# Optimization experiments

Measured on AMD Instinct MI355X. Metric: run time of the kernel, lower is better.

Reference implementation:

```python
import jax, jax.numpy as jnp
import numpy as np

N, E, D, L = 50000, 800000, 128, 2
EPS = 1e-7

def _logmap0(y):
    # Poincare ball (c=1) logmap at origin: artanh(||y||) * y / ||y||
    n = jnp.linalg.norm(y, axis=-1, keepdims=True)
    nc = jnp.clip(n, EPS, 1.0 - 1e-5)
    return jnp.arctanh(nc) * y / jnp.maximum(n, EPS)

def _expmap0(u):
    # Poincare ball (c=1) expmap at origin: tanh(||u||) * u / ||u||
    n = jnp.linalg.norm(u, axis=-1, keepdims=True)
    return jnp.tanh(n) * u / jnp.maximum(n, EPS)

def _l2norm(x):
    # F.normalize(p=2, dim=1)
    return x / jnp.maximum(jnp.linalg.norm(x, axis=1, keepdims=True), 1e-12)

def setup_inputs() -> dict:
    key = jax.random.key(0)
    ks = jax.random.split(key, 12)
    src = jax.random.randint(ks[0], (E,), 0, N)
    dst = jax.random.randint(ks[1], (E,), 0, N)
    e_emb = jax.random.normal(ks[2], (N, D), jnp.float32)
    b_emb = jax.random.normal(ks[3], (N, D), jnp.float32) * 0.1  # inside Poincare ball
    s_emb = jax.random.normal(ks[4], (N, D), jnp.float32)
    sc = 0.05
    eW = jax.random.normal(ks[5], (L, D, D), jnp.float32) * sc
    eB = jax.random.normal(ks[6], (L, D), jnp.float32) * sc
    bW = jax.random.normal(ks[7], (L, D, D), jnp.float32) * sc
    bB = jax.random.normal(ks[8], (L, D), jnp.float32) * sc
    sW = jax.random.normal(ks[9], (L, D, D), jnp.float32) * sc
    sB = jax.random.normal(ks[10], (L, D), jnp.float32) * sc
    return dict(e_emb=e_emb, b_emb=b_emb, s_emb=s_emb, eW=eW, eB=eB,
                bW=bW, bB=bB, sW=sW, sB=sB, src=src, dst=dst)

def reference(e_emb, b_emb, s_emb, eW, eB, bW, bB, sW, sB, src, dst):
    n_nodes = e_emb.shape[0]
    ones_e = jnp.ones(src.shape[0], jnp.float32)
    in_deg = jax.ops.segment_sum(ones_e, dst, num_segments=n_nodes)
    out_deg = jax.ops.segment_sum(ones_e, src, num_segments=n_nodes)
    # DGL GraphConv norm='both': D_out^{-1/2} (sum over in-neighbors) D_in^{-1/2}
    norm_out = jnp.where(out_deg > 0, out_deg ** -0.5, 0.0)[:, None]
    norm_in = jnp.where(in_deg > 0, in_deg ** -0.5, 0.0)[:, None]
    inv_in = jnp.where(in_deg > 0, 1.0 / in_deg, 0.0)[:, None]  # mean reduce

    def agg_sum(h):
        return jax.ops.segment_sum(h[src], dst, num_segments=n_nodes)

    for l in range(L):
        # Euclidean branch: GraphConv(norm='both') then LeakyReLU(0.2)
        h = agg_sum(e_emb * norm_out) * norm_in
        e_emb = jax.nn.leaky_relu(h @ eW[l].T + eB[l], negative_slope=0.2)
        # Hyperbolic branch: logmap0 -> Linear -> neighbor mean -> expmap0
        tan_b = _logmap0(b_emb) @ bW[l].T + bB[l]
        b_emb = _expmap0(agg_sum(tan_b) * inv_in)
        # Spherical branch: normalize -> Linear -> neighbor mean -> normalize
        tan_s = _l2norm(s_emb) @ sW[l].T + sB[l]
        s_emb = _l2norm(agg_sum(tan_s) * inv_in)
    return (e_emb, b_emb, s_emb)
```

## Files before the change

### kernel.cpp

```cpp
#include <hip/hip_runtime.h>
#include <math.h>

#define DD 128
#define PSTRIDE 384

typedef _Float16 half8 __attribute__((ext_vector_type(8)));
typedef _Float16 half2v __attribute__((ext_vector_type(2)));
typedef float floatx4 __attribute__((ext_vector_type(4)));

__device__ __forceinline__ float wave_sum_f(float x) {
#pragma unroll
  for (int m = 32; m >= 1; m >>= 1) x += __shfl_xor(x, m, 64);
  return x;
}
__device__ __forceinline__ float g16_sum(float x) {
#pragma unroll
  for (int m = 8; m >= 1; m >>= 1) x += __shfl_xor(x, m, 64);
  return x;
}
__device__ __forceinline__ int wave_sum_i(int x) {
#pragma unroll
  for (int m = 32; m >= 1; m >>= 1) x += __shfl_xor(x, m, 64);
  return x;
}

__global__ void setup_fused_kernel(const int* __restrict__ src, const int* __restrict__ dst,
                                   int* __restrict__ out_deg, int* __restrict__ in_deg, int E,
                                   const float* __restrict__ e0, const float* __restrict__ b0,
                                   const float* __restrict__ s0, _Float16* __restrict__ P, int N,
                                   const float* __restrict__ eW, const float* __restrict__ bW,
                                   const float* __restrict__ sW, _Float16* __restrict__ Wh, int nW,
                                   int DB, int AB) {
  int bx = blockIdx.x;
  if (bx < DB) {
    int e = bx * 256 + threadIdx.x;
    if (e < E) {
      atomicAdd(&out_deg[src[e]], 1);
      atomicAdd(&in_deg[dst[e]], 1);
    }
  } else if (bx < DB + AB) {
    int lane = threadIdx.x & 63;
    int v = (bx - DB) * 4 + (threadIdx.x >> 6);
    if (v >= N) return;
    size_t ri = (size_t)v * 64 + lane;
    float2 e2 = ((const float2*)e0)[ri];
    float2 b2 = ((const float2*)b0)[ri];
    float2 s2 = ((const float2*)s0)[ri];
    float nb = sqrtf(wave_sum_f(b2.x * b2.x + b2.y * b2.y));
    float ns = sqrtf(wave_sum_f(s2.x * s2.x + s2.y * s2.y));
    float ncb = fminf(fmaxf(nb, 1e-7f), 1.0f - 1e-5f);
    float fb = atanhf(ncb) / fmaxf(nb, 1e-7f);
    float fs = 1.0f / fmaxf(ns, 1e-12f);
    _Float16* Pr = P + (size_t)v * PSTRIDE + lane * 2;
    half2v he; he.x = (_Float16)e2.x;        he.y = (_Float16)e2.y;
    half2v hb; hb.x = (_Float16)(b2.x * fb); hb.y = (_Float16)(b2.y * fb);
    half2v hs; hs.x = (_Float16)(s2.x * fs); hs.y = (_Float16)(s2.y * fs);
    *(half2v*)&Pr[0]   = he;
    *(half2v*)&Pr[128] = hb;
    *(half2v*)&Pr[256] = hs;
  } else {
    int i = (bx - DB - AB) * 256 + threadIdx.x;
    if (i < nW) {
      Wh[i]          = (_Float16)eW[i];
      Wh[i + nW]     = (_Float16)bW[i];
      Wh[i + 2 * nW] = (_Float16)sW[i];
    }
  }
}

__global__ void norms_psum_kernel(const int* __restrict__ in_deg, const int* __restrict__ out_deg,
                                  float* __restrict__ norm_in, float* __restrict__ norm_out,
                                  float* __restrict__ inv_in, int* __restrict__ part, int N) {
  __shared__ int wsum[4];
  int t = threadIdx.x, lane = t & 63, w = t >> 6;
  int i = blockIdx.x * 256 + t;
  int di = 0;
  if (i < N) {
    di = in_deg[i];
    int dq = out_deg[i];
    norm_in[i]  = di > 0 ? 1.0f / sqrtf((float)di) : 0.0f;
    norm_out[i] = dq > 0 ? 1.0f / sqrtf((float)dq) : 0.0f;
    inv_in[i]   = di > 0 ? 1.0f / (float)di : 0.0f;
  }
  int s = wave_sum_i(di);
  if (lane == 0) wsum[w] = s;
  __syncthreads();
  if (t == 0) part[blockIdx.x] = wsum[0] + wsum[1] + wsum[2] + wsum[3];
}

__global__ void part_scan_kernel(int* __restrict__ part, int nb) {
  __shared__ int wsum[4];
  int t = threadIdx.x, lane = t & 63, w = t >> 6;
  int x = (t < nb) ? part[t] : 0;
  int v = x;
#pragma unroll
  for (int off = 1; off < 64; off <<= 1) {
    int y = __shfl_up(v, off, 64);
    if (lane >= off) v += y;
  }
  if (lane == 63) wsum[w] = v;
  __syncthreads();
  int base = 0;
  for (int j = 0; j < w; ++j) base += wsum[j];
  if (t < nb) part[t] = base + v - x;
}

__global__ void local_scan_kernel(const int* __restrict__ deg, const int* __restrict__ part,
                                  int* __restrict__ row_off, int N, int E) {
  __shared__ int wsum[4];
  int t = threadIdx.x, lane = t & 63, w = t >> 6;
  int i = blockIdx.x * 256 + t;
  int x = (i < N) ? deg[i] : 0;
  int v = x;
#pragma unroll
  for (int off = 1; off < 64; off <<= 1) {
    int y = __shfl_up(v, off, 64);
    if (lane >= off) v += y;
  }
  if (lane == 63) wsum[w] = v;
  __syncthreads();
  int base = 0;
  for (int j = 0; j < w; ++j) base += wsum[j];
  if (i < N) row_off[i] = part[blockIdx.x] + base + v - x;
  if (blockIdx.x == 0 && t == 0) row_off[N] = E;
}

__device__ __forceinline__ void gemm_tile(int part, int rb, const _Float16* __restrict__ P,
                                          const _Float16* __restrict__ Wh,
                                          const float* __restrict__ Bb,
                                          _Float16* __restrict__ Q, int N) {
  int t = threadIdx.x, lane = t & 63, w = t >> 6;
  int m = lane & 15, quad = lane >> 4, c0 = w * 32;
  int rbase = rb * 64;
  const _Float16* Ain = P + part * DD;
  _Float16* Qo = Q + part * DD;
  half8 bf[2][4];
#pragma unroll
  for (int tj = 0; tj < 2; ++tj)
#pragma unroll
    for (int kk = 0; kk < 4; ++kk)
      bf[tj][kk] = *(const half8*)&Wh[(c0 + tj * 16 + m) * DD + kk * 32 + quad * 8];
  float bias0 = 0.f, bias1 = 0.f;
  if (Bb) { bias0 = Bb[c0 + m]; bias1 = Bb[c0 + 16 + m]; }
#pragma unroll
  for (int r = 0; r < 4; ++r) {
    int row0 = r * 16;
    int arow = rbase + row0 + m; if (arow >= N) arow = N - 1;
    const _Float16* Ap = Ain + (size_t)arow * PSTRIDE;
    floatx4 acc0 = {0.f, 0.f, 0.f, 0.f}, acc1 = {0.f, 0.f, 0.f, 0.f};
#pragma unroll
    for (int kk = 0; kk < 4; ++kk) {
      half8 af = *(const half8*)&Ap[kk * 32 + quad * 8];
      acc0 = __builtin_amdgcn_mfma_f32_16x16x32_f16(af, bf[0][kk], acc0, 0, 0, 0);
      acc1 = __builtin_amdgcn_mfma_f32_16x16x32_f16(af, bf[1][kk], acc1, 0, 0, 0);
    }
    int vrow = rbase + row0 + quad * 4;
#pragma unroll
    for (int reg = 0; reg < 4; ++reg) {
      int v = vrow + reg;
      if (v < N) {
        Qo[(size_t)v * PSTRIDE + c0 + m]      = (_Float16)(acc0[reg] + bias0);
        Qo[(size_t)v * PSTRIDE + c0 + 16 + m] = (_Float16)(acc1[reg] + bias1);
      }
    }
  }
}

__global__ __launch_bounds__(256) void fill_gemm_kernel(
    const int* __restrict__ src, const int* __restrict__ dst,
    const float* __restrict__ norm_out, const int* __restrict__ row_off,
    int* __restrict__ cursor, int2* __restrict__ csr_sw, int E,
    const _Float16* __restrict__ P, const _Float16* __restrict__ WhE,
    const _Float16* __restrict__ WhB, const _Float16* __restrict__ WhS,
    const float* __restrict__ bBl, const float* __restrict__ sBl,
    _Float16* __restrict__ Q, int N, int FB, int GB) {
  int bx = blockIdx.x;
  if (bx < FB) {
    int e = bx * 256 + threadIdx.x;
    if (e < E) {
      int d = dst[e], s = src[e];
      int pos = row_off[d] + atomicAdd(&cursor[d], 1);
      csr_sw[pos] = make_int2(s, __float_as_int(norm_out[s]));
    }
  } else {
    int gb = bx - FB;
    int part = gb / GB, rb = gb % GB;
    const _Float16* Wh = (part == 0) ? WhE : (part == 1 ? WhB : WhS);
    const float* Bb = (part == 0) ? nullptr : (part == 1 ? bBl : sBl);
    gemm_tile(part, rb, P, Wh, Bb, Q, N);
  }
}

__global__ __launch_bounds__(256) void gemm3_kernel(const _Float16* __restrict__ P,
                                                    const _Float16* __restrict__ WhE,
                                                    const _Float16* __restrict__ WhB,
                                                    const _Float16* __restrict__ WhS,
                                                    const float* __restrict__ bBl,
                                                    const float* __restrict__ sBl,
                                                    _Float16* __restrict__ Q, int N) {
  int part = blockIdx.y;
  const _Float16* Wh = (part == 0) ? WhE : (part == 1 ? WhB : WhS);
  const float* Bb = (part == 0) ? nullptr : (part == 1 ? bBl : sBl);
  gemm_tile(part, blockIdx.x, P, Wh, Bb, Q, N);
}

__global__ __launch_bounds__(256) void agg_fused_kernel(
    const _Float16* __restrict__ Q, const int* __restrict__ row_off,
    const int2* __restrict__ csr_sw, const float* __restrict__ norm_in,
    const float* __restrict__ inv_in, const float* __restrict__ eBias,
    float* __restrict__ oe, float* __restrict__ ob, float* __restrict__ os,
    _Float16* __restrict__ Pnext, int N, int write_pack, int write_out) {
  int lane = threadIdx.x & 63;
  int v = blockIdx.x * 4 + (threadIdx.x >> 6);
  if (v >= N) return;
  int g = lane >> 4, q = lane & 15;
  int beg = row_off[v], end = row_off[v + 1];
  float eacc[8], bacc[8], sacc[8];
#pragma unroll
  for (int j = 0; j < 8; ++j) { eacc[j] = 0.f; bacc[j] = 0.f; sacc[j] = 0.f; }
  int i = beg;
  for (; i + 8 <= end; i += 8) {
    int2 swa = csr_sw[i + g];
    int2 swb = csr_sw[i + 4 + g];
    float wa = __int_as_float(swa.y), wb = __int_as_float(swb.y);
    const _Float16* ra = Q + (size_t)swa.x * PSTRIDE + q * 8;
    const _Float16* rb = Q + (size_t)swb.x * PSTRIDE + q * 8;
    half8 ea = *(const half8*)ra;
    half8 e2 = *(const half8*)rb;
    half8 ba = *(const half8*)(ra + 128);
    half8 b2 = *(const half8*)(rb + 128);
    half8 sa = *(const half8*)(ra + 256);
    half8 s2 = *(const half8*)(rb + 256);
#pragma unroll
    for (int j = 0; j < 8; ++j) {
      eacc[j] += wa * (float)ea[j];
      eacc[j] += wb * (float)e2[j];
      bacc[j] += (float)ba[j];
      bacc[j] += (float)b2[j];
      sacc[j] += (float)sa[j];
      sacc[j] += (float)s2[j];
    }
  }
  if (i + 4 <= end) {
    int2 sw = csr_sw[i + g];
    float wgt = __int_as_float(sw.y);
    const _Float16* rp = Q + (size_t)sw.x * PSTRIDE + q * 8;
    half8 ev = *(const half8*)rp;
    half8 bv = *(const half8*)(rp + 128);
    half8 sv = *(const half8*)(rp + 256);
#pragma unroll
    for (int j = 0; j < 8; ++j) {
      eacc[j] += wgt * (float)ev[j];
      bacc[j] += (float)bv[j];
      sacc[j] += (float)sv[j];
    }
    i += 4;
  }
  if (i + g < end) {
    int2 sw = csr_sw[i + g];
    float wgt = __int_as_float(sw.y);
    const _Float16* rp = Q + (size_t)sw.x * PSTRIDE + q * 8;
    half8 ev = *(const half8*)rp;
    half8 bv = *(const half8*)(rp + 128);
    half8 sv = *(const half8*)(rp + 256);
#pragma unroll
    for (int j = 0; j < 8; ++j) {
      eacc[j] += wgt * (float)ev[j];
      bacc[j] += (float)bv[j];
      sacc[j] += (float)sv[j];
    }
  }
#pragma unroll
  for (int j = 0; j < 8; ++j) {
    eacc[j] += __shfl_xor(eacc[j], 16, 64);
    eacc[j] += __shfl_xor(eacc[j], 32, 64);
    bacc[j] += __shfl_xor(bacc[j], 16, 64);
    bacc[j] += __shfl_xor(bacc[j], 32, 64);
    sacc[j] += __shfl_xor(sacc[j], 16, 64);
    sacc[j] += __shfl_xor(sacc[j], 32, 64);
  }
  float ni = norm_in[v], iv = inv_in[v];
  const float4* ebp = (const float4*)eBias;
  float4 eb0 = ebp[q * 2], eb1 = ebp[q * 2 + 1];
  float bias[8] = {eb0.x, eb0.y, eb0.z, eb0.w, eb1.x, eb1.y, eb1.z, eb1.w};
  float h[8], ub[8], us[8];
  float ss2 = 0.f;
#pragma unroll
  for (int j = 0; j < 8; ++j) {
    float t = eacc[j] * ni + bias[j];
    h[j] = t > 0.f ? t : 0.2f * t;
    ub[j] = bacc[j] * iv;
    us[j] = sacc[j] * iv; ss2 += us[j] * us[j];
  }
  float ns = sqrtf(g16_sum(ss2));
  float fs = 1.0f / fmaxf(ns, 1e-12f);
  if (write_out) {
    float bs2 = 0.f;
#pragma unroll
    for (int j = 0; j < 8; ++j) bs2 += ub[j] * ub[j];
    float nb = sqrtf(g16_sum(bs2));
    float fb = tanhf(nb) / fmaxf(nb, 1e-7f);
    if (g == 0) {
      float4* p = (float4*)(oe + (size_t)v * DD);
      p[q * 2]     = make_float4(h[0], h[1], h[2], h[3]);
      p[q * 2 + 1] = make_float4(h[4], h[5], h[6], h[7]);
    } else if (g == 1) {
      float4* p = (float4*)(ob + (size_t)v * DD);
      p[q * 2]     = make_float4(ub[0] * fb, ub[1] * fb, ub[2] * fb, ub[3] * fb);
      p[q * 2 + 1] = make_float4(ub[4] * fb, ub[5] * fb, ub[6] * fb, ub[7] * fb);
    } else if (g == 2) {
      float4* p = (float4*)(os + (size_t)v * DD);
      p[q * 2]     = make_float4(us[0] * fs, us[1] * fs, us[2] * fs, us[3] * fs);
      p[q * 2 + 1] = make_float4(us[4] * fs, us[5] * fs, us[6] * fs, us[7] * fs);
    }
  }
  if (write_pack) {
    if (g == 3) {
      half8 he, hb, hs;
#pragma unroll
      for (int j = 0; j < 8; ++j) {
        he[j] = (_Float16)h[j];
        hb[j] = (_Float16)ub[j];
        hs[j] = (_Float16)(us[j] * fs);
      }
      _Float16* Pr = Pnext + (size_t)v * PSTRIDE + q * 8;
      *(half8*)&Pr[0]   = he;
      *(half8*)&Pr[128] = hb;
      *(half8*)&Pr[256] = hs;
    }
  }
}

extern "C" void kernel_launch(void* const* d_in, const int* in_sizes, int n_in,
                              void* d_out, int out_size, void* d_ws, size_t ws_size,
                              hipStream_t stream) {
  const float* e0 = (const float*)d_in[0];
  const float* b0 = (const float*)d_in[1];
  const float* s0 = (const float*)d_in[2];
  const float* eW = (const float*)d_in[3];
  const float* eB = (const float*)d_in[4];
  const float* bW = (const float*)d_in[5];
  const float* bB = (const float*)d_in[6];
  const float* sW = (const float*)d_in[7];
  const float* sB = (const float*)d_in[8];
  const int* src = (const int*)d_in[9];
  const int* dst = (const int*)d_in[10];
  int N = in_sizes[0] / DD;
  int E = in_sizes[9];
  int L = in_sizes[3] / (DD * DD);
  int LDD2 = L * DD * DD;

  char* w = (char*)d_ws;
  int* in_deg  = (int*)w; w += (size_t)N * 4;
  int* out_deg = (int*)w; w += (size_t)N * 4;
  int* cursor  = (int*)w; w += (size_t)N * 4;
  int* row_off = (int*)w; w += (size_t)(N + 4) * 4;
  int* pscan   = (int*)w; w += (size_t)1024 * 4;
  int2* csr_sw = (int2*)w; w += (size_t)E * 8;
  float* norm_in  = (float*)w; w += (size_t)N * 4;
  float* norm_out = (float*)w; w += (size_t)N * 4;
  float* inv_in   = (float*)w; w += (size_t)N * 4;
  w = (char*)(((size_t)w + 255) & ~(size_t)255);
  _Float16* P = (_Float16*)w; w += (size_t)N * PSTRIDE * 2;
  _Float16* Q = (_Float16*)w; w += (size_t)N * PSTRIDE * 2;
  _Float16* Wh = (_Float16*)w; w += (size_t)3 * LDD2 * 2;
  _Float16* whE = Wh;
  _Float16* whB = Wh + LDD2;
  _Float16* whS = Wh + 2 * LDD2;

  float* oe = (float*)d_out;
  float* ob = oe + (size_t)N * DD;
  float* os = ob + (size_t)N * DD;

  int DB = (E + 255) / 256;
  int AB = (N + 3) / 4;
  int GB = (N + 63) / 64;
  int WB = (LDD2 + 255) / 256;
  int PB = (N + 255) / 256;

  hipMemsetAsync(d_ws, 0, (size_t)3 * N * 4, stream);
  setup_fused_kernel<<<DB + AB + WB, 256, 0, stream>>>(src, dst, out_deg, in_deg, E,
                                                       e0, b0, s0, P, N,
                                                       eW, bW, sW, Wh, LDD2, DB, AB);
  norms_psum_kernel<<<PB, 256, 0, stream>>>(in_deg, out_deg, norm_in, norm_out, inv_in, pscan, N);
  part_scan_kernel<<<1, 256, 0, stream>>>(pscan, PB);
  local_scan_kernel<<<PB, 256, 0, stream>>>(in_deg, pscan, row_off, N, E);
  fill_gemm_kernel<<<DB + 3 * GB, 256, 0, stream>>>(src, dst, norm_out, row_off, cursor, csr_sw, E,
                                                    P, whE, whB, whS, bB, sB, Q, N, DB, GB);
  agg_fused_kernel<<<AB, 256, 0, stream>>>(Q, row_off, csr_sw, norm_in, inv_in, eB,
                                           oe, ob, os, P, N,
                                           (L > 1) ? 1 : 0, (L == 1) ? 1 : 0);
  for (int l = 1; l < L; ++l) {
    size_t lo = (size_t)l * DD * DD;
    gemm3_kernel<<<dim3(GB, 3), 256, 0, stream>>>(P, whE + lo, whB + lo, whS + lo,
                                                  bB + (size_t)l * DD, sB + (size_t)l * DD, Q, N);
    agg_fused_kernel<<<AB, 256, 0, stream>>>(Q, row_off, csr_sw, norm_in, inv_in,
                                             eB + (size_t)l * DD, oe, ob, os, P, N,
                                             (l < L - 1) ? 1 : 0, (l == L - 1) ? 1 : 0);
  }
}
```

Baseline: 496.2 us.

## Fuse layer-0 input prep into GEMM and spread degree atomics over 8 copies

The separate pass that converted the fp32 inputs to fp16 and applied logmap0 or l2 normalisation into P is removed. The first GEMM now reads fp32 rows directly, computes each row's norm inside the tile, and applies the per-row scale to the MFMA output before the bias. Degree counting now spreads atomics across 8 histogram copies chosen by wave index, and the norms kernel sums those copies. This cuts a full-size read and write pass and atomic contention, at the cost of a larger memset and more fp32 loads in the GEMM.

```diff
diff --git a/kernel.cpp b/kernel.cpp
--- a/kernel.cpp
+++ b/kernel.cpp
@@ -5,61 +5,35 @@
 #define PSTRIDE 384
 
 typedef _Float16 half8 __attribute__((ext_vector_type(8)));
-typedef _Float16 half2v __attribute__((ext_vector_type(2)));
 typedef float floatx4 __attribute__((ext_vector_type(4)));
 
-__device__ __forceinline__ float wave_sum_f(float x) {
+__device__ __forceinline__ float g16_sum(float x) {
+#pragma unroll
+  for (int m = 8; m >= 1; m >>= 1) x += __shfl_xor(x, m, 64);
+  return x;
+}
+__device__ __forceinline__ int wave_sum_i(int x) {
 #pragma unroll
   for (int m = 32; m >= 1; m >>= 1) x += __shfl_xor(x, m, 64);
   return x;
 }
-__device__ __forceinline__ float g16_sum(float x) {
-#pragma unroll
-  for (int m = 8; m >= 1; m >>= 1) x += __shfl_xor(x, m, 64);
-  return x;
-}
-__device__ __forceinline__ int wave_sum_i(int x) {
-#pragma unroll
-  for (int m = 32; m >= 1; m >>= 1) x += __shfl_xor(x, m, 64);
-  return x;
-}
-
-__global__ void setup_fused_kernel(const int* __restrict__ src, const int* __restrict__ dst,
-                                   int* __restrict__ out_deg, int* __restrict__ in_deg, int E,
-                                   const float* __restrict__ e0, const float* __restrict__ b0,
-                                   const float* __restrict__ s0, _Float16* __restrict__ P, int N,
-                                   const float* __restrict__ eW, const float* __restrict__ bW,
-                                   const float* __restrict__ sW, _Float16* __restrict__ Wh, int nW,
-                                   int DB, int AB) {
+
+__global__ void deg_wcvt_kernel(const int* __restrict__ src, const int* __restrict__ dst,
+                                int* __restrict__ out_deg8, int* __restrict__ in_deg8,
+                                int E, int N,
+                                const float* __restrict__ eW, const float* __restrict__ bW,
+                                const float* __restrict__ sW, _Float16* __restrict__ Wh, int nW,
+                                int DB) {
   int bx = blockIdx.x;
   if (bx < DB) {
     int e = bx * 256 + threadIdx.x;
     if (e < E) {
-      atomicAdd(&out_deg[src[e]], 1);
-      atomicAdd(&in_deg[dst[e]], 1);
-    }
-  } else if (bx < DB + AB) {
-    int lane = threadIdx.x & 63;
-    int v = (bx - DB) * 4 + (threadIdx.x >> 6);
-    if (v >= N) return;
-    size_t ri = (size_t)v * 64 + lane;
-    float2 e2 = ((const float2*)e0)[ri];
-    float2 b2 = ((const float2*)b0)[ri];
-    float2 s2 = ((const float2*)s0)[ri];
-    float nb = sqrtf(wave_sum_f(b2.x * b2.x + b2.y * b2.y));
-    float ns = sqrtf(wave_sum_f(s2.x * s2.x + s2.y * s2.y));
-    float ncb = fminf(fmaxf(nb, 1e-7f), 1.0f - 1e-5f);
-    float fb = atanhf(ncb) / fmaxf(nb, 1e-7f);
-    float fs = 1.0f / fmaxf(ns, 1e-12f);
-    _Float16* Pr = P + (size_t)v * PSTRIDE + lane * 2;
-    half2v he; he.x = (_Float16)e2.x;        he.y = (_Float16)e2.y;
-    half2v hb; hb.x = (_Float16)(b2.x * fb); hb.y = (_Float16)(b2.y * fb);
-    half2v hs; hs.x = (_Float16)(s2.x * fs); hs.y = (_Float16)(s2.y * fs);
-    *(half2v*)&Pr[0]   = he;
-    *(half2v*)&Pr[128] = hb;
-    *(half2v*)&Pr[256] = hs;
+      int h = ((bx << 2) + (threadIdx.x >> 6)) & 7;
+      atomicAdd(&out_deg8[h * N + src[e]], 1);
+      atomicAdd(&in_deg8[h * N + dst[e]], 1);
+    }
   } else {
-    int i = (bx - DB - AB) * 256 + threadIdx.x;
+    int i = (bx - DB) * 256 + threadIdx.x;
     if (i < nW) {
       Wh[i]          = (_Float16)eW[i];
       Wh[i + nW]     = (_Float16)bW[i];
@@ -68,16 +42,22 @@
   }
 }
 
-__global__ void norms_psum_kernel(const int* __restrict__ in_deg, const int* __restrict__ out_deg,
-                                  float* __restrict__ norm_in, float* __restrict__ norm_out,
-                                  float* __restrict__ inv_in, int* __restrict__ part, int N) {
+__global__ void norms_psum_kernel(const int* __restrict__ in_deg8, const int* __restrict__ out_deg8,
+                                  int* __restrict__ in_deg, float* __restrict__ norm_in,
+                                  float* __restrict__ norm_out, float* __restrict__ inv_in,
+                                  int* __restrict__ part, int N) {
   __shared__ int wsum[4];
   int t = threadIdx.x, lane = t & 63, w = t >> 6;
   int i = blockIdx.x * 256 + t;
   int di = 0;
   if (i < N) {
-    di = in_deg[i];
-    int dq = out_deg[i];
+    int dq = 0;
+#pragma unroll
+    for (int h = 0; h < 8; ++h) {
+      di += in_deg8[h * N + i];
+      dq += out_deg8[h * N + i];
+    }
+    in_deg[i] = di;
     norm_in[i]  = di > 0 ? 1.0f / sqrtf((float)di) : 0.0f;
     norm_out[i] = dq > 0 ? 1.0f / sqrtf((float)dq) : 0.0f;
     inv_in[i]   = di > 0 ? 1.0f / (float)di : 0.0f;
@@ -123,6 +103,72 @@
   for (int j = 0; j < w; ++j) base += wsum[j];
   if (i < N) row_off[i] = part[blockIdx.x] + base + v - x;
   if (blockIdx.x == 0 && t == 0) row_off[N] = E;
+}
+
+__device__ __forceinline__ void gemm0_tile(int part, int rb, const float* __restrict__ A,
+                                           const _Float16* __restrict__ Wh,
+                                           const float* __restrict__ Bb,
+                                           _Float16* __restrict__ Q, int N) {
+  int t = threadIdx.x, lane = t & 63, w = t >> 6;
+  int m = lane & 15, quad = lane >> 4, c0 = w * 32;
+  int rbase = rb * 64;
+  _Float16* Qo = Q + part * DD;
+  half8 bf[2][4];
+#pragma unroll
+  for (int tj = 0; tj < 2; ++tj)
+#pragma unroll
+    for (int kk = 0; kk < 4; ++kk)
+      bf[tj][kk] = *(const half8*)&Wh[(c0 + tj * 16 + m) * DD + kk * 32 + quad * 8];
+  float bias0 = 0.f, bias1 = 0.f;
+  if (part) { bias0 = Bb[c0 + m]; bias1 = Bb[c0 + 16 + m]; }
+#pragma unroll
+  for (int r = 0; r < 4; ++r) {
+    int row0 = r * 16;
+    int arow = rbase + row0 + m; if (arow >= N) arow = N - 1;
+    const float* Ap = A + (size_t)arow * DD;
+    half8 af[4];
+    float nsq = 0.f;
+#pragma unroll
+    for (int kk = 0; kk < 4; ++kk) {
+      float4 x0 = *(const float4*)&Ap[kk * 32 + quad * 8];
+      float4 x1 = *(const float4*)&Ap[kk * 32 + quad * 8 + 4];
+      if (part)
+        nsq += x0.x * x0.x + x0.y * x0.y + x0.z * x0.z + x0.w * x0.w +
+               x1.x * x1.x + x1.y * x1.y + x1.z * x1.z + x1.w * x1.w;
+      half8 a;
+      a[0] = (_Float16)x0.x; a[1] = (_Float16)x0.y; a[2] = (_Float16)x0.z; a[3] = (_Float16)x0.w;
+      a[4] = (_Float16)x1.x; a[5] = (_Float16)x1.y; a[6] = (_Float16)x1.z; a[7] = (_Float16)x1.w;
+      af[kk] = a;
+    }
+    float fr = 1.f;
+    if (part) {
+      nsq += __shfl_xor(nsq, 16, 64);
+      nsq += __shfl_xor(nsq, 32, 64);
+      float n = sqrtf(nsq);
+      if (part == 1) {
+        float nc = fminf(fmaxf(n, 1e-7f), 1.0f - 1e-5f);
+        fr = atanhf(nc) / fmaxf(n, 1e-7f);
+      } else {
+        fr = 1.0f / fmaxf(n, 1e-12f);
+      }
+    }
+    floatx4 acc0 = {0.f, 0.f, 0.f, 0.f}, acc1 = {0.f, 0.f, 0.f, 0.f};
+#pragma unroll
+    for (int kk = 0; kk < 4; ++kk) {
+      acc0 = __builtin_amdgcn_mfma_f32_16x16x32_f16(af[kk], bf[0][kk], acc0, 0, 0, 0);
+      acc1 = __builtin_amdgcn_mfma_f32_16x16x32_f16(af[kk], bf[1][kk], acc1, 0, 0, 0);
+    }
+    int vrow = rbase + row0 + quad * 4;
+#pragma unroll
+    for (int reg = 0; reg < 4; ++reg) {
+      int v = vrow + reg;
+      float fs = part ? __shfl(fr, quad * 4 + reg, 64) : 1.f;
+      if (v < N) {
+        Qo[(size_t)v * PSTRIDE + c0 + m]      = (_Float16)(acc0[reg] * fs + bias0);
+        Qo[(size_t)v * PSTRIDE + c0 + 16 + m] = (_Float16)(acc1[reg] * fs + bias1);
+      }
+    }
+  }
 }
 
 __device__ __forceinline__ void gemm_tile(int part, int rb, const _Float16* __restrict__ P,
@@ -166,14 +212,14 @@
   }
 }
 
-__global__ __launch_bounds__(256) void fill_gemm_kernel(
+__global__ __launch_bounds__(256) void fill_gemm0_kernel(
     const int* __restrict__ src, const int* __restrict__ dst,
     const float* __restrict__ norm_out, const int* __restrict__ row_off,
     int* __restrict__ cursor, int2* __restrict__ csr_sw, int E,
-    const _Float16* __restrict__ P, const _Float16* __restrict__ WhE,
-    const _Float16* __restrict__ WhB, const _Float16* __restrict__ WhS,
-    const float* __restrict__ bBl, const float* __restrict__ sBl,
-    _Float16* __restrict__ Q, int N, int FB, int GB) {
+    const float* __restrict__ e0, const float* __restrict__ b0, const float* __restrict__ s0,
+    const _Float16* __restrict__ WhE, const _Float16* __restrict__ WhB,
+    const _Float16* __restrict__ WhS, const float* __restrict__ bBl,
+    const float* __restrict__ sBl, _Float16* __restrict__ Q, int N, int FB, int GB) {
   int bx = blockIdx.x;
   if (bx < FB) {
     int e = bx * 256 + threadIdx.x;
@@ -185,9 +231,10 @@
   } else {
     int gb = bx - FB;
     int part = gb / GB, rb = gb % GB;
+    const float* A = (part == 0) ? e0 : (part == 1 ? b0 : s0);
     const _Float16* Wh = (part == 0) ? WhE : (part == 1 ? WhB : WhS);
     const float* Bb = (part == 0) ? nullptr : (part == 1 ? bBl : sBl);
-    gemm_tile(part, rb, P, Wh, Bb, Q, N);
+    gemm0_tile(part, rb, A, Wh, Bb, Q, N);
   }
 }
 
@@ -351,12 +398,13 @@
   int LDD2 = L * DD * DD;
 
   char* w = (char*)d_ws;
-  int* in_deg  = (int*)w; w += (size_t)N * 4;
-  int* out_deg = (int*)w; w += (size_t)N * 4;
-  int* cursor  = (int*)w; w += (size_t)N * 4;
-  int* row_off = (int*)w; w += (size_t)(N + 4) * 4;
-  int* pscan   = (int*)w; w += (size_t)1024 * 4;
-  int2* csr_sw = (int2*)w; w += (size_t)E * 8;
+  int* in_deg8  = (int*)w; w += (size_t)8 * N * 4;
+  int* out_deg8 = (int*)w; w += (size_t)8 * N * 4;
+  int* cursor   = (int*)w; w += (size_t)N * 4;
+  int* in_deg   = (int*)w; w += (size_t)N * 4;
+  int* row_off  = (int*)w; w += (size_t)(N + 4) * 4;
+  int* pscan    = (int*)w; w += (size_t)1024 * 4;
+  int2* csr_sw  = (int2*)w; w += (size_t)E * 8;
   float* norm_in  = (float*)w; w += (size_t)N * 4;
   float* norm_out = (float*)w; w += (size_t)N * 4;
   float* inv_in   = (float*)w; w += (size_t)N * 4;
@@ -378,15 +426,16 @@
   int WB = (LDD2 + 255) / 256;
   int PB = (N + 255) / 256;
 
-  hipMemsetAsync(d_ws, 0, (size_t)3 * N * 4, stream);
-  setup_fused_kernel<<<DB + AB + WB, 256, 0, stream>>>(src, dst, out_deg, in_deg, E,
-                                                       e0, b0, s0, P, N,
-                                                       eW, bW, sW, Wh, LDD2, DB, AB);
-  norms_psum_kernel<<<PB, 256, 0, stream>>>(in_deg, out_deg, norm_in, norm_out, inv_in, pscan, N);
+  hipMemsetAsync(d_ws, 0, (size_t)17 * N * 4, stream);
+  deg_wcvt_kernel<<<DB + WB, 256, 0, stream>>>(src, dst, out_deg8, in_deg8, E, N,
+                                               eW, bW, sW, Wh, LDD2, DB);
+  norms_psum_kernel<<<PB, 256, 0, stream>>>(in_deg8, out_deg8, in_deg,
+                                            norm_in, norm_out, inv_in, pscan, N);
   part_scan_kernel<<<1, 256, 0, stream>>>(pscan, PB);
   local_scan_kernel<<<PB, 256, 0, stream>>>(in_deg, pscan, row_off, N, E);
-  fill_gemm_kernel<<<DB + 3 * GB, 256, 0, stream>>>(src, dst, norm_out, row_off, cursor, csr_sw, E,
-                                                    P, whE, whB, whS, bB, sB, Q, N, DB, GB);
+  fill_gemm0_kernel<<<DB + 3 * GB, 256, 0, stream>>>(src, dst, norm_out, row_off, cursor,
+                                                     csr_sw, E, e0, b0, s0,
+                                                     whE, whB, whS, bB, sB, Q, N, DB, GB);
   agg_fused_kernel<<<AB, 256, 0, stream>>>(Q, row_off, csr_sw, norm_in, inv_in, eB,
                                            oe, ob, os, P, N,
                                            (L > 1) ? 1 : 0, (L == 1) ? 1 : 0);
```

New measurement: 494.2 us. About the same (-0.4%).
